# Kernel tuning notes

Measured on AMD Instinct MI355X. Metric: run time of the kernel, lower is better.

## Reference

```python
import jax, jax.numpy as jnp
import numpy as np

U = 359347   # user_num (hardcoded in source)
I = 292589   # item_num (hardcoded in source)
D = 64       # factor_num
NNZ = 4_000_000
B = 32768
LAM = 0.001  # lamada


def setup_inputs() -> dict:
    key = jax.random.key(0)
    ks = jax.random.split(key, 19)
    return {
        "ui_rows": jax.random.randint(ks[0], (NNZ,), 0, U, dtype=jnp.int32),
        "ui_cols": jax.random.randint(ks[1], (NNZ,), 0, I, dtype=jnp.int32),
        "ui_vals": jax.random.uniform(ks[2], (NNZ,), dtype=jnp.float32),
        "iu_vals": jax.random.uniform(ks[3], (NNZ,), dtype=jnp.float32),
        "d_i": jax.random.uniform(ks[4], (U,), dtype=jnp.float32),
        "d_j": jax.random.uniform(ks[5], (I,), dtype=jnp.float32),
        "embed_user": jax.random.normal(ks[6], (U, D), dtype=jnp.float32) * 0.01,
        "embed_item": jax.random.normal(ks[7], (I, D), dtype=jnp.float32) * 0.01,
        "add_w": jax.random.normal(ks[8], (1, 3), dtype=jnp.float32),
        "fw1": jax.random.normal(ks[9], (2 * D, D), dtype=jnp.float32) * (1.0 / np.sqrt(D)),
        "fb1": jax.random.normal(ks[10], (2 * D,), dtype=jnp.float32) * 0.01,
        "fw2": jax.random.normal(ks[11], (D, 2 * D), dtype=jnp.float32) * (1.0 / np.sqrt(2 * D)),
        "fb2": jax.random.normal(ks[12], (D,), dtype=jnp.float32) * 0.01,
        "user_bias": jax.random.normal(ks[13], (U, 1), dtype=jnp.float32) * 0.01,
        "item_bias": jax.random.normal(ks[14], (I, 1), dtype=jnp.float32) * 0.01,
        "avg_rating": jax.random.uniform(ks[15], (1,), dtype=jnp.float32) * 5.0,
        "user0": jax.random.randint(ks[16], (B,), 0, U, dtype=jnp.int32),
        "item_i0": jax.random.randint(ks[17], (B,), 0, I, dtype=jnp.int32),
        "ratings": jax.random.uniform(ks[18], (B,), dtype=jnp.float32) * 5.0,
    }


def _spmm(rows, cols, vals, x, num_rows):
    # sparse [num_rows, *] COO @ dense x : gather rows of x by col index,
    # scale by edge value, scatter-add into destination rows.
    return jax.ops.segment_sum(vals[:, None] * x[cols], rows, num_segments=num_rows)


def _leaky(x):
    return jnp.where(x > 0, x, 0.1 * x)


def _user_filter(x, fw1, fb1, fw2, fb2):
    h = _leaky(x @ fw1.T + fb1)
    return _leaky(h @ fw2.T + fb2)


def reference(ui_rows, ui_cols, ui_vals, iu_vals, d_i, d_j,
              embed_user, embed_item, add_w, fw1, fb1, fw2, fb2,
              user_bias, item_bias, avg_rating, user0, item_i0, ratings):
    ue, ie = embed_user, embed_item
    # layer 1: SpMM + degree-scaled residual + ReLU
    g1_u = jax.nn.relu(_spmm(ui_rows, ui_cols, ui_vals, ie, U) + ue * d_i[:, None])
    g1_i = jax.nn.relu(_spmm(ui_cols, ui_rows, iu_vals, ue, I) + ie * d_j[:, None])
    # layer 2
    g2_u = jax.nn.relu(_spmm(ui_rows, ui_cols, ui_vals, g1_i, U) + g1_u * d_i[:, None])
    g2_i = jax.nn.relu(_spmm(ui_cols, ui_rows, iu_vals, g1_u, I) + g1_i * d_j[:, None])
    # learned combination of the 3 layers: Linear(3,1) over the stacked axis
    w = add_w[0]  # [3]
    gcn_u = w[0] * ue + w[1] * g1_u + w[2] * g2_u   # [U, D]
    gcn_i = w[0] * ie + w[1] * g1_i + w[2] * g2_i   # [I, D]
    # batch lookup + shared filter MLP
    user = _user_filter(gcn_u[user0], fw1, fb1, fw2, fb2)      # [B, D]
    item = _user_filter(gcn_i[item_i0], fw1, fb1, fw2, fb2)    # [B, D]
    pred = (user * item).sum(-1) + user_bias[user0, 0] + item_bias[item_i0, 0] + avg_rating
    l2 = LAM * jnp.mean(gcn_u ** 2) + LAM * jnp.mean(gcn_i ** 2)
    loss2 = jnp.mean((pred - ratings) ** 2)
    return loss2 + l2
```

## Files before the change

kernel.cpp:

```cpp
#include <hip/hip_runtime.h>

#define U_NUM 359347
#define I_NUM 292589
#define DDIM  64
#define NNZ_N 4000000
#define BATCH 32768
#define LAM_F 0.001f
#define ACC_SLOTS 2048

#define EPB   4096
#define NBLK  ((NNZ_N + EPB - 1) / EPB)
#define NB_U  ((U_NUM + 1023) >> 10)
#define NB_I  ((I_NUM + 1023) >> 10)

__device__ __forceinline__ float leaky(float x) { return x > 0.f ? x : 0.1f * x; }

__device__ __forceinline__ unsigned short f2bf(float f) {
    unsigned b = __float_as_uint(f);
    b = (b + 0x7FFF + ((b >> 16) & 1)) >> 16;
    return (unsigned short)b;
}
__device__ __forceinline__ float bf2f(unsigned short u) {
    return __uint_as_float((unsigned)u << 16);
}
__device__ __forceinline__ float bflo(unsigned u) { return __uint_as_float(u << 16); }
__device__ __forceinline__ float bfhi(unsigned u) { return __uint_as_float(u & 0xffff0000u); }

__device__ __forceinline__ unsigned char f2fp8(float v) {
    v = fminf(fmaxf(v * 64.f, -440.f), 440.f);
    unsigned b = __float_as_uint(v * 0x1p-120f);
    unsigned sign = (b >> 24) & 0x80u;
    unsigned mag = b & 0x7fffffffu;
    mag += 0x7ffffu + ((mag >> 20) & 1u);
    return (unsigned char)(sign | ((mag >> 20) & 0x7fu));
}

#if __has_builtin(__builtin_amdgcn_cvt_f32_fp8)
#define FP8DEC(b) __builtin_amdgcn_cvt_f32_fp8((int)(b), 0)
#else
#define FP8DEC(b) (__uint_as_float(((unsigned)((b) & 0x80u) << 24) | \
                                   ((unsigned)((b) & 0x7fu) << 20)) * 0x1p120f)
#endif

__global__ __launch_bounds__(256) void f2bf8_k(
    const float4* __restrict__ in, ushort4* __restrict__ outb,
    uchar4* __restrict__ out8, size_t n4)
{
    size_t stride = (size_t)gridDim.x * 256;
    for (size_t i = (size_t)blockIdx.x * 256 + threadIdx.x; i < n4; i += stride) {
        float4 v = in[i];
        ushort4 o;
        o.x = f2bf(v.x); o.y = f2bf(v.y); o.z = f2bf(v.z); o.w = f2bf(v.w);
        outb[i] = o;
        uchar4 p;
        p.x = f2fp8(v.x); p.y = f2fp8(v.y); p.z = f2fp8(v.z); p.w = f2fp8(v.w);
        out8[i] = p;
    }
}

__global__ __launch_bounds__(256) void l1hist_k(
    const int* __restrict__ keys, int* __restrict__ gh, int nb)
{
    __shared__ int h[512];
    for (int i = threadIdx.x; i < nb; i += 256) h[i] = 0;
    __syncthreads();
    int base = blockIdx.x * EPB;
    int end = min(base + EPB, NNZ_N);
    for (int e = base + threadIdx.x; e < end; e += 256)
        atomicAdd(&h[keys[e] >> 10], 1);
    __syncthreads();
    for (int i = threadIdx.x; i < nb; i += 256)
        gh[i * NBLK + blockIdx.x] = h[i];
}

__global__ __launch_bounds__(256) void scan1_k(int* __restrict__ a, int n, int* __restrict__ bsum)
{
    __shared__ int s[256];
    int t = threadIdx.x;
    int base = blockIdx.x * 1024 + t * 4;
    int v[4];
#pragma unroll
    for (int j = 0; j < 4; ++j) v[j] = (base + j < n) ? a[base + j] : 0;
    s[t] = v[0] + v[1] + v[2] + v[3];
    __syncthreads();
    for (int off = 1; off < 256; off <<= 1) {
        int x = (t >= off) ? s[t - off] : 0;
        __syncthreads();
        s[t] += x;
        __syncthreads();
    }
    if (t == 255) bsum[blockIdx.x] = s[255];
    int run = (t > 0) ? s[t - 1] : 0;
#pragma unroll
    for (int j = 0; j < 4; ++j) {
        if (base + j < n) a[base + j] = run;
        run += v[j];
    }
}

__global__ __launch_bounds__(512) void scan2_k(int* __restrict__ bsum, int nb)
{
    __shared__ int s[512];
    int t = threadIdx.x;
    int v = (t < nb) ? bsum[t] : 0;
    s[t] = v;
    __syncthreads();
    for (int off = 1; off < 512; off <<= 1) {
        int x = (t >= off) ? s[t - off] : 0;
        __syncthreads();
        s[t] += x;
        __syncthreads();
    }
    if (t < nb) bsum[t] = s[t] - v;
}

__global__ __launch_bounds__(256) void scan3_k(int* __restrict__ a, int n,
                                               const int* __restrict__ bsum)
{
    int add = bsum[blockIdx.x];
    int base = blockIdx.x * 1024 + threadIdx.x * 4;
#pragma unroll
    for (int j = 0; j < 4; ++j)
        if (base + j < n) a[base + j] += add;
}

__global__ __launch_bounds__(256) void l1scatter_k(
    const int* __restrict__ keys, const int* __restrict__ gh, int nb,
    int2* __restrict__ out)
{
    __shared__ int cur[512];
    for (int i = threadIdx.x; i < nb; i += 256) cur[i] = gh[i * NBLK + blockIdx.x];
    __syncthreads();
    int base = blockIdx.x * EPB;
    int end = min(base + EPB, NNZ_N);
    for (int e = base + threadIdx.x; e < end; e += 256) {
        int k = keys[e];
        int pos = atomicAdd(&cur[k >> 10], 1);
        out[pos] = make_int2(k, e);
    }
}

__global__ __launch_bounds__(256) void l2sort_k(
    const int2* __restrict__ tmp, const int* __restrict__ gh, int nb,
    const int* __restrict__ colArr, const float* __restrict__ valArr,
    int* __restrict__ ptr, int nrows,
    int* __restrict__ ecol, unsigned short* __restrict__ eval)
{
    __shared__ int hist[1024];
    __shared__ int ssc[256];
    int b = blockIdx.x;
    int t = threadIdx.x;
    int bucket_base = gh[b * NBLK];
    int bucket_end  = (b == nb - 1) ? NNZ_N : gh[(b + 1) * NBLK];
    for (int i = t; i < 1024; i += 256) hist[i] = 0;
    __syncthreads();
    for (int e = bucket_base + t; e < bucket_end; e += 256)
        atomicAdd(&hist[tmp[e].x & 1023], 1);
    __syncthreads();
    int v0 = hist[t * 4], v1 = hist[t * 4 + 1], v2 = hist[t * 4 + 2], v3 = hist[t * 4 + 3];
    ssc[t] = v0 + v1 + v2 + v3;
    __syncthreads();
    for (int off = 1; off < 256; off <<= 1) {
        int x = (t >= off) ? ssc[t - off] : 0;
        __syncthreads();
        ssc[t] += x;
        __syncthreads();
    }
    int run = (t > 0) ? ssc[t - 1] : 0;
    int g0 = run, g1 = run + v0, g2 = g1 + v1, g3 = g2 + v2;
    hist[t * 4] = g0; hist[t * 4 + 1] = g1; hist[t * 4 + 2] = g2; hist[t * 4 + 3] = g3;
    int rbase = b << 10;
    if (rbase + t * 4 < nrows)     ptr[rbase + t * 4]     = bucket_base + g0;
    if (rbase + t * 4 + 1 < nrows) ptr[rbase + t * 4 + 1] = bucket_base + g1;
    if (rbase + t * 4 + 2 < nrows) ptr[rbase + t * 4 + 2] = bucket_base + g2;
    if (rbase + t * 4 + 3 < nrows) ptr[rbase + t * 4 + 3] = bucket_base + g3;
    if (b == nb - 1 && t == 0) ptr[nrows] = NNZ_N;
    __syncthreads();
    for (int e = bucket_base + t; e < bucket_end; e += 256) {
        int2 q = tmp[e];
        int pos = bucket_base + atomicAdd(&hist[q.x & 1023], 1);
        ecol[pos] = colArr[q.y];
        eval[pos] = f2bf(valArr[q.y] * 0.015625f);
    }
}

template <int MODE>
__global__ __launch_bounds__(256) void spmm_csr_k(
    const int* __restrict__ ptr, const int* __restrict__ ecol,
    const unsigned short* __restrict__ eval,
    const unsigned char* __restrict__ x8, const unsigned short* base,
    const float* __restrict__ deg, unsigned short* out, int nrows,
    unsigned char* __restrict__ out8,
    const unsigned short* embed, const float* __restrict__ add_w,
    float* __restrict__ accArr)
{
    int wv = threadIdx.x >> 6, lane = threadIdx.x & 63;
    int r = blockIdx.x * 4 + wv;
    __shared__ float ssum[4];
    if (r < nrows) {
        int s0 = __builtin_amdgcn_readfirstlane(ptr[r]);
        int e0 = __builtin_amdgcn_readfirstlane(ptr[r + 1]);
        float a0 = 0.f, a1 = 0.f, a2 = 0.f, a3 = 0.f;
        int k = s0;
        for (; k + 4 <= e0; k += 4) {
            int c0 = ecol[k], c1 = ecol[k + 1], c2 = ecol[k + 2], c3 = ecol[k + 3];
            float v0 = bf2f(eval[k]),     v1 = bf2f(eval[k + 1]);
            float v2 = bf2f(eval[k + 2]), v3 = bf2f(eval[k + 3]);
            unsigned char b0 = x8[(size_t)c0 * DDIM + lane];
            unsigned char b1 = x8[(size_t)c1 * DDIM + lane];
            unsigned char b2 = x8[(size_t)c2 * DDIM + lane];
            unsigned char b3 = x8[(size_t)c3 * DDIM + lane];
            a0 = fmaf(v0, FP8DEC(b0), a0);
            a1 = fmaf(v1, FP8DEC(b1), a1);
            a2 = fmaf(v2, FP8DEC(b2), a2);
            a3 = fmaf(v3, FP8DEC(b3), a3);
        }
        for (; k < e0; ++k)
            a0 = fmaf(bf2f(eval[k]), FP8DEC(x8[(size_t)ecol[k] * DDIM + lane]), a0);
        float acc = (a0 + a1) + (a2 + a3);
        float bb = bf2f(base[(size_t)r * DDIM + lane]);
        float o = fmaxf(fmaf(bb, deg[r], acc), 0.f);
        if (MODE == 0) {
            out[(size_t)r * DDIM + lane] = f2bf(o);
            out8[(size_t)r * DDIM + lane] = f2fp8(o);
        } else {
            float g = fmaf(add_w[0], bf2f(embed[(size_t)r * DDIM + lane]),
                           fmaf(add_w[1], bb, add_w[2] * o));
            out[(size_t)r * DDIM + lane] = f2bf(g);
            float sq = g * g;
            for (int off = 32; off; off >>= 1) sq += __shfl_down(sq, off);
            if (lane == 0) ssum[wv] = sq;
        }
    } else if (MODE == 1) {
        if (lane == 0) ssum[wv] = 0.f;
    }
    if (MODE == 1) {
        __syncthreads();
        if (threadIdx.x == 0)
            atomicAdd(&accArr[blockIdx.x & (ACC_SLOTS - 1)],
                      ssum[0] + ssum[1] + ssum[2] + ssum[3]);
    }
}

__global__ __launch_bounds__(256) void mlp_k(
    const int* __restrict__ user0, const int* __restrict__ item0,
    const unsigned short* __restrict__ gcnU, const unsigned short* __restrict__ gcnI,
    const float* __restrict__ fw1, const float* __restrict__ fb1,
    const float* __restrict__ fw2, const float* __restrict__ fb2,
    unsigned short* __restrict__ ou, unsigned short* __restrict__ oi)
{
    __shared__ unsigned short xs[64][72];
    __shared__ unsigned short w1s[128][68];
    __shared__ unsigned short w2s[64][140];
    __shared__ unsigned short hs[128][72];
    __shared__ float b1s[128];
    __shared__ float b2s[64];

    int t = threadIdx.x;
    int side = blockIdx.x >> 9;
    int tile = blockIdx.x & 511;
    const int* sel = side ? item0 : user0;
    const unsigned short* gcn = side ? gcnI : gcnU;
    unsigned short* outp = side ? oi : ou;

    {
        int r = t >> 2, c = t & 3;
        int idx = sel[tile * 64 + r];
        const ushort4* src = (const ushort4*)(gcn + (size_t)idx * 64 + c * 16);
        ushort4 v0 = src[0], v1 = src[1], v2 = src[2], v3 = src[3];
        int k0 = c * 16;
        xs[k0 +  0][r] = v0.x; xs[k0 +  1][r] = v0.y; xs[k0 +  2][r] = v0.z; xs[k0 +  3][r] = v0.w;
        xs[k0 +  4][r] = v1.x; xs[k0 +  5][r] = v1.y; xs[k0 +  6][r] = v1.z; xs[k0 +  7][r] = v1.w;
        xs[k0 +  8][r] = v2.x; xs[k0 +  9][r] = v2.y; xs[k0 + 10][r] = v2.z; xs[k0 + 11][r] = v2.w;
        xs[k0 + 12][r] = v3.x; xs[k0 + 13][r] = v3.y; xs[k0 + 14][r] = v3.z; xs[k0 + 15][r] = v3.w;
    }
#pragma unroll
    for (int i = 0; i < 8; ++i) {
        int flat = i * 1024 + t * 4;
        float4 w = *(const float4*)(fw1 + flat);
        int o = flat >> 6, k = flat & 63;
        *(unsigned*)&w1s[o][k]     = (unsigned)f2bf(w.x) | ((unsigned)f2bf(w.y) << 16);
        *(unsigned*)&w1s[o][k + 2] = (unsigned)f2bf(w.z) | ((unsigned)f2bf(w.w) << 16);
        float4 u = *(const float4*)(fw2 + flat);
        int o2 = flat >> 7, k2 = flat & 127;
        *(unsigned*)&w2s[o2][k2]     = (unsigned)f2bf(u.x) | ((unsigned)f2bf(u.y) << 16);
        *(unsigned*)&w2s[o2][k2 + 2] = (unsigned)f2bf(u.z) | ((unsigned)f2bf(u.w) << 16);
    }
    if (t < 128) b1s[t] = fb1[t];
    if (t < 64)  b2s[t] = fb2[t];
    __syncthreads();

    int sg = t & 15, og = t >> 4;

    float acc[4][8];
#pragma unroll
    for (int i = 0; i < 4; ++i)
#pragma unroll
        for (int j = 0; j < 8; ++j) acc[i][j] = 0.f;

    for (int kc = 0; kc < 64; kc += 4) {
        uint2 xp0 = *(const uint2*)&xs[kc    ][sg * 4];
        uint2 xp1 = *(const uint2*)&xs[kc + 1][sg * 4];
        uint2 xp2 = *(const uint2*)&xs[kc + 2][sg * 4];
        uint2 xp3 = *(const uint2*)&xs[kc + 3][sg * 4];
        float x0[4] = { bflo(xp0.x), bfhi(xp0.x), bflo(xp0.y), bfhi(xp0.y) };
        float x1[4] = { bflo(xp1.x), bfhi(xp1.x), bflo(xp1.y), bfhi(xp1.y) };
        float x2[4] = { bflo(xp2.x), bfhi(xp2.x), bflo(xp2.y), bfhi(xp2.y) };
        float x3[4] = { bflo(xp3.x), bfhi(xp3.x), bflo(xp3.y), bfhi(xp3.y) };
#pragma unroll
        for (int j = 0; j < 8; ++j) {
            uint2 wp = *(const uint2*)&w1s[og * 8 + j][kc];
            float w0 = bflo(wp.x), w1v = bfhi(wp.x), w2v = bflo(wp.y), w3v = bfhi(wp.y);
#pragma unroll
            for (int i = 0; i < 4; ++i) {
                acc[i][j] = fmaf(x0[i], w0,  acc[i][j]);
                acc[i][j] = fmaf(x1[i], w1v, acc[i][j]);
                acc[i][j] = fmaf(x2[i], w2v, acc[i][j]);
                acc[i][j] = fmaf(x3[i], w3v, acc[i][j]);
            }
        }
    }
#pragma unroll
    for (int j = 0; j < 8; ++j) {
        int o = og * 8 + j;
        float b = b1s[o];
        float h0 = leaky(acc[0][j] + b), h1 = leaky(acc[1][j] + b);
        float h2 = leaky(acc[2][j] + b), h3 = leaky(acc[3][j] + b);
        *(unsigned*)&hs[o][sg * 4]     = (unsigned)f2bf(h0) | ((unsigned)f2bf(h1) << 16);
        *(unsigned*)&hs[o][sg * 4 + 2] = (unsigned)f2bf(h2) | ((unsigned)f2bf(h3) << 16);
    }
    __syncthreads();

    float acc2[4][4];
#pragma unroll
    for (int i = 0; i < 4; ++i)
#pragma unroll
        for (int j = 0; j < 4; ++j) acc2[i][j] = 0.f;

    for (int kc = 0; kc < 128; kc += 4) {
        uint2 hp0 = *(const uint2*)&hs[kc    ][sg * 4];
        uint2 hp1 = *(const uint2*)&hs[kc + 1][sg * 4];
        uint2 hp2 = *(const uint2*)&hs[kc + 2][sg * 4];
        uint2 hp3 = *(const uint2*)&hs[kc + 3][sg * 4];
        float h0[4] = { bflo(hp0.x), bfhi(hp0.x), bflo(hp0.y), bfhi(hp0.y) };
        float h1[4] = { bflo(hp1.x), bfhi(hp1.x), bflo(hp1.y), bfhi(hp1.y) };
        float h2[4] = { bflo(hp2.x), bfhi(hp2.x), bflo(hp2.y), bfhi(hp2.y) };
        float h3[4] = { bflo(hp3.x), bfhi(hp3.x), bflo(hp3.y), bfhi(hp3.y) };
#pragma unroll
        for (int j = 0; j < 4; ++j) {
            uint2 wp = *(const uint2*)&w2s[og * 4 + j][kc];
            float w0 = bflo(wp.x), w1v = bfhi(wp.x), w2v = bflo(wp.y), w3v = bfhi(wp.y);
#pragma unroll
            for (int i = 0; i < 4; ++i) {
                acc2[i][j] = fmaf(h0[i], w0,  acc2[i][j]);
                acc2[i][j] = fmaf(h1[i], w1v, acc2[i][j]);
                acc2[i][j] = fmaf(h2[i], w2v, acc2[i][j]);
                acc2[i][j] = fmaf(h3[i], w3v, acc2[i][j]);
            }
        }
    }
#pragma unroll
    for (int i = 0; i < 4; ++i) {
        float o0 = leaky(acc2[i][0] + b2s[og * 4 + 0]);
        float o1 = leaky(acc2[i][1] + b2s[og * 4 + 1]);
        float o2 = leaky(acc2[i][2] + b2s[og * 4 + 2]);
        float o3 = leaky(acc2[i][3] + b2s[og * 4 + 3]);
        uint2 pp;
        pp.x = (unsigned)f2bf(o0) | ((unsigned)f2bf(o1) << 16);
        pp.y = (unsigned)f2bf(o2) | ((unsigned)f2bf(o3) << 16);
        *(uint2*)(outp + ((size_t)(tile * 64 + sg * 4 + i) * 64 + og * 4)) = pp;
    }
}

__global__ __launch_bounds__(256) void dot_sse_k(
    const unsigned short* __restrict__ ou, const unsigned short* __restrict__ oi,
    const int* __restrict__ user0, const int* __restrict__ item0,
    const float* __restrict__ ub, const float* __restrict__ ib,
    const float* __restrict__ avg, const float* __restrict__ ratings,
    float* __restrict__ sse)
{
    int g = blockIdx.x * 256 + threadIdx.x;
    int b = g >> 2, q = g & 3;
    const uint4* pu = (const uint4*)(ou + (size_t)b * 64 + q * 16);
    const uint4* pi = (const uint4*)(oi + (size_t)b * 64 + q * 16);
    uint4 a0 = pu[0], a1 = pu[1];
    uint4 c0 = pi[0], c1 = pi[1];
    float s = 0.f;
#define DOTP(ua, uc) { s = fmaf(bflo(ua), bflo(uc), s); s = fmaf(bfhi(ua), bfhi(uc), s); }
    DOTP(a0.x, c0.x) DOTP(a0.y, c0.y) DOTP(a0.z, c0.z) DOTP(a0.w, c0.w)
    DOTP(a1.x, c1.x) DOTP(a1.y, c1.y) DOTP(a1.z, c1.z) DOTP(a1.w, c1.w)
#undef DOTP
    s += __shfl_xor(s, 1);
    s += __shfl_xor(s, 2);
    float contrib = 0.f;
    if (q == 0) {
        float pred = s + ub[user0[b]] + ib[item0[b]] + avg[0];
        float d = pred - ratings[b];
        contrib = d * d;
    }
    for (int off = 32; off; off >>= 1) contrib += __shfl_down(contrib, off);
    __shared__ float wsum[4];
    int lane = threadIdx.x & 63, wv = threadIdx.x >> 6;
    if (lane == 0) wsum[wv] = contrib;
    __syncthreads();
    if (threadIdx.x == 0)
        atomicAdd(sse, wsum[0] + wsum[1] + wsum[2] + wsum[3]);
}

__global__ __launch_bounds__(256) void finalize2_k(
    const float* __restrict__ accU, const float* __restrict__ accI,
    const float* __restrict__ sse, float* __restrict__ out)
{
    int t = threadIdx.x;
    float su = 0.f, si = 0.f;
    for (int i = t; i < ACC_SLOTS; i += 256) { su += accU[i]; si += accI[i]; }
    for (int off = 32; off; off >>= 1) {
        su += __shfl_down(su, off);
        si += __shfl_down(si, off);
    }
    __shared__ float s[8];
    int wv = t >> 6, lane = t & 63;
    if (lane == 0) { s[wv] = su; s[wv + 4] = si; }
    __syncthreads();
    if (t == 0) {
        float SU = s[0] + s[1] + s[2] + s[3];
        float SI = s[4] + s[5] + s[6] + s[7];
        out[0] = sse[0] / (float)BATCH
               + LAM_F * (SU / (float)((double)U_NUM * 64.0))
               + LAM_F * (SI / (float)((double)I_NUM * 64.0));
    }
}


extern "C" void kernel_launch(void* const* d_in, const int* in_sizes, int n_in,
                              void* d_out, int out_size, void* d_ws, size_t ws_size,
                              hipStream_t stream)
{
    const int*   ui_rows = (const int*)d_in[0];
    const int*   ui_cols = (const int*)d_in[1];
    const float* ui_vals = (const float*)d_in[2];
    const float* iu_vals = (const float*)d_in[3];
    const float* d_i     = (const float*)d_in[4];
    const float* d_j     = (const float*)d_in[5];
    const float* eu      = (const float*)d_in[6];
    const float* ei      = (const float*)d_in[7];
    const float* add_w   = (const float*)d_in[8];
    const float* fw1     = (const float*)d_in[9];
    const float* fb1     = (const float*)d_in[10];
    const float* fw2     = (const float*)d_in[11];
    const float* fb2     = (const float*)d_in[12];
    const float* ub      = (const float*)d_in[13];
    const float* ib      = (const float*)d_in[14];
    const float* avg     = (const float*)d_in[15];
    const int*   user0   = (const int*)d_in[16];
    const int*   item0   = (const int*)d_in[17];
    const float* ratings = (const float*)d_in[18];

    const size_t U64 = (size_t)U_NUM * DDIM;
    const size_t I64 = (size_t)I_NUM * DDIM;

    int*            ecol_u = (int*)d_ws;
    unsigned short* eval_u = (unsigned short*)(ecol_u + NNZ_N);
    int*            ecol_i = (int*)(eval_u + NNZ_N);
    unsigned short* eval_i = (unsigned short*)(ecol_i + NNZ_N);
    int2* tmpb  = (int2*)(eval_i + NNZ_N);
    unsigned char*  g1u_f8 = (unsigned char*)tmpb;
    unsigned short* ou_bf  = (unsigned short*)(g1u_f8 + ((U64 + 15) & ~15ull));
    unsigned short* oi_bf  = ou_bf + (size_t)BATCH * 64;
    int*  gh    = (int*)(tmpb + NNZ_N);
    int*  bsum  = gh + (size_t)NB_U * NBLK;
    int*  ptr_u = bsum + 512;
    int*  ptr_i = ptr_u + (U_NUM + 1);
    float* accU = (float*)(ptr_i + (I_NUM + 1));
    float* accI = accU + ACC_SLOTS;
    float* sse  = accI + ACC_SLOTS;
    unsigned short* eu_bf  = (unsigned short*)(sse + 4);
    unsigned short* ei_bf  = eu_bf + U64;
    unsigned short* g1u_bf = ei_bf + I64;
    unsigned short* g1i_bf = g1u_bf + U64;
    unsigned char*  eu_f8  = (unsigned char*)(g1i_bf + I64);
    unsigned char*  ei_f8  = eu_f8 + U64;
    unsigned char*  g1i_f8 = ei_f8 + I64;
    (void)ws_size;

    dim3 blk(256);
    int gu = (U_NUM + 3) / 4, gi = (I_NUM + 3) / 4;

    hipMemsetAsync(accU, 0, (2 * ACC_SLOTS + 4) * sizeof(float), stream);

    f2bf8_k<<<2048, blk, 0, stream>>>((const float4*)eu, (ushort4*)eu_bf,
                                      (uchar4*)eu_f8, U64 / 4);
    f2bf8_k<<<2048, blk, 0, stream>>>((const float4*)ei, (ushort4*)ei_bf,
                                      (uchar4*)ei_f8, I64 / 4);

    {
        int n = NB_U * NBLK;
        int nb1 = (n + 1023) / 1024;
        l1hist_k<<<NBLK, blk, 0, stream>>>(ui_rows, gh, NB_U);
        scan1_k<<<nb1, blk, 0, stream>>>(gh, n, bsum);
        scan2_k<<<1, 512, 0, stream>>>(bsum, nb1);
        scan3_k<<<nb1, blk, 0, stream>>>(gh, n, bsum);
        l1scatter_k<<<NBLK, blk, 0, stream>>>(ui_rows, gh, NB_U, tmpb);
        l2sort_k<<<NB_U, blk, 0, stream>>>(tmpb, gh, NB_U, ui_cols, ui_vals,
                                           ptr_u, U_NUM, ecol_u, eval_u);
    }
    {
        int n = NB_I * NBLK;
        int nb1 = (n + 1023) / 1024;
        l1hist_k<<<NBLK, blk, 0, stream>>>(ui_cols, gh, NB_I);
        scan1_k<<<nb1, blk, 0, stream>>>(gh, n, bsum);
        scan2_k<<<1, 512, 0, stream>>>(bsum, nb1);
        scan3_k<<<nb1, blk, 0, stream>>>(gh, n, bsum);
        l1scatter_k<<<NBLK, blk, 0, stream>>>(ui_cols, gh, NB_I, tmpb);
        l2sort_k<<<NB_I, blk, 0, stream>>>(tmpb, gh, NB_I, ui_rows, iu_vals,
                                           ptr_i, I_NUM, ecol_i, eval_i);
    }

    spmm_csr_k<0><<<gu, blk, 0, stream>>>(ptr_u, ecol_u, eval_u, ei_f8, eu_bf, d_i,
                                          g1u_bf, U_NUM, g1u_f8, nullptr, nullptr, nullptr);
    spmm_csr_k<0><<<gi, blk, 0, stream>>>(ptr_i, ecol_i, eval_i, eu_f8, ei_bf, d_j,
                                          g1i_bf, I_NUM, g1i_f8, nullptr, nullptr, nullptr);
    spmm_csr_k<1><<<gi, blk, 0, stream>>>(ptr_i, ecol_i, eval_i, g1u_f8, g1i_bf, d_j,
                                          ei_bf, I_NUM, nullptr, ei_bf, add_w, accI);
    spmm_csr_k<1><<<gu, blk, 0, stream>>>(ptr_u, ecol_u, eval_u, g1i_f8, g1u_bf, d_i,
                                          g1u_bf, U_NUM, nullptr, eu_bf, add_w, accU);

    mlp_k<<<1024, blk, 0, stream>>>(user0, item0, g1u_bf, ei_bf,
                                    fw1, fb1, fw2, fb2, ou_bf, oi_bf);
    dot_sse_k<<<BATCH * 4 / 256, blk, 0, stream>>>(ou_bf, oi_bf, user0, item0,
                                                   ub, ib, avg, ratings, sse);
    finalize2_k<<<1, blk, 0, stream>>>(accU, accI, sse, (float*)d_out);
}
```

Measured before the change: 1.323 ms.

## Merge user/item preprocessing and SpMM launches, carry col/val through scatter

Independent user-side and item-side kernels are merged into single launches that pick their side by block index. This covers the embedding conversion, histogram, the three scan stages and both SpMM layers. The first-level scatter now writes the column index and the pre-scaled bf16 value alongside the key. The second-level sort then copies them sequentially instead of doing random gathers into the original column and value arrays. The SpMM inner loop is unrolled to 8 edges to keep more gather loads in flight. The cost is an extra temporary value buffer, larger per-side histogram and workspace arrays, and some per-block selection overhead and register pressure.

```diff
diff --git a/kernel.cpp b/kernel.cpp
--- a/kernel.cpp
+++ b/kernel.cpp
@@ -34,7 +34,6 @@
     mag += 0x7ffffu + ((mag >> 20) & 1u);
     return (unsigned char)(sign | ((mag >> 20) & 0x7fu));
 }
-
 #if __has_builtin(__builtin_amdgcn_cvt_f32_fp8)
 #define FP8DEC(b) __builtin_amdgcn_cvt_f32_fp8((int)(b), 0)
 #else
@@ -43,41 +42,58 @@
 #endif
 
 __global__ __launch_bounds__(256) void f2bf8_k(
-    const float4* __restrict__ in, ushort4* __restrict__ outb,
-    uchar4* __restrict__ out8, size_t n4)
+    const float4* __restrict__ inU, ushort4* __restrict__ obU, uchar4* __restrict__ o8U,
+    const float4* __restrict__ inI, ushort4* __restrict__ obI, uchar4* __restrict__ o8I,
+    size_t nU4, size_t total4)
 {
     size_t stride = (size_t)gridDim.x * 256;
-    for (size_t i = (size_t)blockIdx.x * 256 + threadIdx.x; i < n4; i += stride) {
-        float4 v = in[i];
+    for (size_t i = (size_t)blockIdx.x * 256 + threadIdx.x; i < total4; i += stride) {
+        const float4* in; ushort4* ob; uchar4* o8; size_t j;
+        if (i < nU4) { in = inU; ob = obU; o8 = o8U; j = i; }
+        else         { in = inI; ob = obI; o8 = o8I; j = i - nU4; }
+        float4 v = in[j];
         ushort4 o;
         o.x = f2bf(v.x); o.y = f2bf(v.y); o.z = f2bf(v.z); o.w = f2bf(v.w);
-        outb[i] = o;
+        ob[j] = o;
         uchar4 p;
         p.x = f2fp8(v.x); p.y = f2fp8(v.y); p.z = f2fp8(v.z); p.w = f2fp8(v.w);
-        out8[i] = p;
-    }
-}
-
-__global__ __launch_bounds__(256) void l1hist_k(
-    const int* __restrict__ keys, int* __restrict__ gh, int nb)
+        o8[j] = p;
+    }
+}
+
+__global__ __launch_bounds__(256) void hist2_k(
+    const int* __restrict__ rows, const int* __restrict__ cols,
+    int* __restrict__ gh_u, int* __restrict__ gh_i)
 {
     __shared__ int h[512];
+    int sideB = blockIdx.x >= NBLK;
+    int blk = sideB ? blockIdx.x - NBLK : blockIdx.x;
+    const int* keys = sideB ? cols : rows;
+    int nb = sideB ? NB_I : NB_U;
+    int* gh = sideB ? gh_i : gh_u;
     for (int i = threadIdx.x; i < nb; i += 256) h[i] = 0;
     __syncthreads();
-    int base = blockIdx.x * EPB;
+    int base = blk * EPB;
     int end = min(base + EPB, NNZ_N);
     for (int e = base + threadIdx.x; e < end; e += 256)
         atomicAdd(&h[keys[e] >> 10], 1);
     __syncthreads();
     for (int i = threadIdx.x; i < nb; i += 256)
-        gh[i * NBLK + blockIdx.x] = h[i];
-}
-
-__global__ __launch_bounds__(256) void scan1_k(int* __restrict__ a, int n, int* __restrict__ bsum)
+        gh[i * NBLK + blk] = h[i];
+}
+
+__global__ __launch_bounds__(256) void scan1m_k(
+    int* __restrict__ aU, int nUe, int* __restrict__ bsU, int nb1U,
+    int* __restrict__ aI, int nIe, int* __restrict__ bsI)
 {
     __shared__ int s[256];
+    int sideB = (int)blockIdx.x >= nb1U;
+    int blk = sideB ? blockIdx.x - nb1U : blockIdx.x;
+    int* a = sideB ? aI : aU;
+    int n = sideB ? nIe : nUe;
+    int* bsum = sideB ? bsI : bsU;
     int t = threadIdx.x;
-    int base = blockIdx.x * 1024 + t * 4;
+    int base = blk * 1024 + t * 4;
     int v[4];
 #pragma unroll
     for (int j = 0; j < 4; ++j) v[j] = (base + j < n) ? a[base + j] : 0;
@@ -89,7 +105,7 @@
         s[t] += x;
         __syncthreads();
     }
-    if (t == 255) bsum[blockIdx.x] = s[255];
+    if (t == 255) bsum[blk] = s[255];
     int run = (t > 0) ? s[t - 1] : 0;
 #pragma unroll
     for (int j = 0; j < 4; ++j) {
@@ -98,9 +114,12 @@
     }
 }
 
-__global__ __launch_bounds__(512) void scan2_k(int* __restrict__ bsum, int nb)
+__global__ __launch_bounds__(512) void scan2m_k(
+    int* __restrict__ bsU, int nbU, int* __restrict__ bsI, int nbI)
 {
     __shared__ int s[512];
+    int* bsum = blockIdx.x ? bsI : bsU;
+    int nb = blockIdx.x ? nbI : nbU;
     int t = threadIdx.x;
     int v = (t < nb) ? bsum[t] : 0;
     s[t] = v;
@@ -114,19 +133,25 @@
     if (t < nb) bsum[t] = s[t] - v;
 }
 
-__global__ __launch_bounds__(256) void scan3_k(int* __restrict__ a, int n,
-                                               const int* __restrict__ bsum)
-{
-    int add = bsum[blockIdx.x];
-    int base = blockIdx.x * 1024 + threadIdx.x * 4;
+__global__ __launch_bounds__(256) void scan3m_k(
+    int* __restrict__ aU, int nUe, const int* __restrict__ bsU, int nb1U,
+    int* __restrict__ aI, int nIe, const int* __restrict__ bsI)
+{
+    int sideB = (int)blockIdx.x >= nb1U;
+    int blk = sideB ? blockIdx.x - nb1U : blockIdx.x;
+    int* a = sideB ? aI : aU;
+    int n = sideB ? nIe : nUe;
+    int add = (sideB ? bsI : bsU)[blk];
+    int base = blk * 1024 + threadIdx.x * 4;
 #pragma unroll
     for (int j = 0; j < 4; ++j)
         if (base + j < n) a[base + j] += add;
 }
 
-__global__ __launch_bounds__(256) void l1scatter_k(
-    const int* __restrict__ keys, const int* __restrict__ gh, int nb,
-    int2* __restrict__ out)
+__global__ __launch_bounds__(256) void scat_k(
+    const int* __restrict__ keys, const int* __restrict__ cols,
+    const float* __restrict__ vals, const int* __restrict__ gh, int nb,
+    int2* __restrict__ tmpb, unsigned short* __restrict__ tmpv)
 {
     __shared__ int cur[512];
     for (int i = threadIdx.x; i < nb; i += 256) cur[i] = gh[i * NBLK + blockIdx.x];
@@ -136,14 +161,14 @@
     for (int e = base + threadIdx.x; e < end; e += 256) {
         int k = keys[e];
         int pos = atomicAdd(&cur[k >> 10], 1);
-        out[pos] = make_int2(k, e);
+        tmpb[pos] = make_int2(k, cols[e]);
+        tmpv[pos] = f2bf(vals[e] * 0.015625f);
     }
 }
 
 __global__ __launch_bounds__(256) void l2sort_k(
-    const int2* __restrict__ tmp, const int* __restrict__ gh, int nb,
-    const int* __restrict__ colArr, const float* __restrict__ valArr,
-    int* __restrict__ ptr, int nrows,
+    const int2* __restrict__ tmpb, const unsigned short* __restrict__ tmpv,
+    const int* __restrict__ gh, int nb, int* __restrict__ ptr, int nrows,
     int* __restrict__ ecol, unsigned short* __restrict__ eval)
 {
     __shared__ int hist[1024];
@@ -155,7 +180,7 @@
     for (int i = t; i < 1024; i += 256) hist[i] = 0;
     __syncthreads();
     for (int e = bucket_base + t; e < bucket_end; e += 256)
-        atomicAdd(&hist[tmp[e].x & 1023], 1);
+        atomicAdd(&hist[tmpb[e].x & 1023], 1);
     __syncthreads();
     int v0 = hist[t * 4], v1 = hist[t * 4 + 1], v2 = hist[t * 4 + 2], v3 = hist[t * 4 + 3];
     ssc[t] = v0 + v1 + v2 + v3;
@@ -177,43 +202,75 @@
     if (b == nb - 1 && t == 0) ptr[nrows] = NNZ_N;
     __syncthreads();
     for (int e = bucket_base + t; e < bucket_end; e += 256) {
-        int2 q = tmp[e];
+        int2 q = tmpb[e];
         int pos = bucket_base + atomicAdd(&hist[q.x & 1023], 1);
-        ecol[pos] = colArr[q.y];
-        eval[pos] = f2bf(valArr[q.y] * 0.015625f);
+        ecol[pos] = q.y;
+        eval[pos] = tmpv[e];
     }
 }
 
 template <int MODE>
-__global__ __launch_bounds__(256) void spmm_csr_k(
-    const int* __restrict__ ptr, const int* __restrict__ ecol,
-    const unsigned short* __restrict__ eval,
-    const unsigned char* __restrict__ x8, const unsigned short* base,
-    const float* __restrict__ deg, unsigned short* out, int nrows,
-    unsigned char* __restrict__ out8,
-    const unsigned short* embed, const float* __restrict__ add_w,
-    float* __restrict__ accArr)
+__global__ __launch_bounds__(256) void spmm_dual_k(
+    int gA,
+    const int* __restrict__ ptrA, const int* __restrict__ ecolA, const unsigned short* __restrict__ evalA,
+    const unsigned char* __restrict__ x8A, const unsigned short* baseA, const float* __restrict__ degA,
+    unsigned short* outA, int nA, unsigned char* __restrict__ out8A,
+    const unsigned short* embedA, float* __restrict__ accA,
+    const int* __restrict__ ptrB, const int* __restrict__ ecolB, const unsigned short* __restrict__ evalB,
+    const unsigned char* __restrict__ x8B, const unsigned short* baseB, const float* __restrict__ degB,
+    unsigned short* outB, int nB, unsigned char* __restrict__ out8B,
+    const unsigned short* embedB, float* __restrict__ accB,
+    const float* __restrict__ add_w)
 {
     int wv = threadIdx.x >> 6, lane = threadIdx.x & 63;
-    int r = blockIdx.x * 4 + wv;
+    int bid = blockIdx.x;
+    int sideB = bid >= gA;
+    int lb = sideB ? bid - gA : bid;
+    const int* ptr = sideB ? ptrB : ptrA;
+    const int* ecol = sideB ? ecolB : ecolA;
+    const unsigned short* eval = sideB ? evalB : evalA;
+    const unsigned char* x8 = sideB ? x8B : x8A;
+    const unsigned short* base = sideB ? baseB : baseA;
+    const float* deg = sideB ? degB : degA;
+    unsigned short* out = sideB ? outB : outA;
+    int nrows = sideB ? nB : nA;
     __shared__ float ssum[4];
+    int r = lb * 4 + wv;
     if (r < nrows) {
         int s0 = __builtin_amdgcn_readfirstlane(ptr[r]);
         int e0 = __builtin_amdgcn_readfirstlane(ptr[r + 1]);
         float a0 = 0.f, a1 = 0.f, a2 = 0.f, a3 = 0.f;
         int k = s0;
-        for (; k + 4 <= e0; k += 4) {
-            int c0 = ecol[k], c1 = ecol[k + 1], c2 = ecol[k + 2], c3 = ecol[k + 3];
-            float v0 = bf2f(eval[k]),     v1 = bf2f(eval[k + 1]);
-            float v2 = bf2f(eval[k + 2]), v3 = bf2f(eval[k + 3]);
+        for (; k + 8 <= e0; k += 8) {
+            int c0 = ecol[k],     c1 = ecol[k + 1], c2 = ecol[k + 2], c3 = ecol[k + 3];
+            int c4 = ecol[k + 4], c5 = ecol[k + 5], c6 = ecol[k + 6], c7 = ecol[k + 7];
             unsigned char b0 = x8[(size_t)c0 * DDIM + lane];
             unsigned char b1 = x8[(size_t)c1 * DDIM + lane];
             unsigned char b2 = x8[(size_t)c2 * DDIM + lane];
             unsigned char b3 = x8[(size_t)c3 * DDIM + lane];
-            a0 = fmaf(v0, FP8DEC(b0), a0);
-            a1 = fmaf(v1, FP8DEC(b1), a1);
-            a2 = fmaf(v2, FP8DEC(b2), a2);
-            a3 = fmaf(v3, FP8DEC(b3), a3);
+            unsigned char b4 = x8[(size_t)c4 * DDIM + lane];
+            unsigned char b5 = x8[(size_t)c5 * DDIM + lane];
+            unsigned char b6 = x8[(size_t)c6 * DDIM + lane];
+            unsigned char b7 = x8[(size_t)c7 * DDIM + lane];
+            a0 = fmaf(bf2f(eval[k]),     FP8DEC(b0), a0);
+            a1 = fmaf(bf2f(eval[k + 1]), FP8DEC(b1), a1);
+            a2 = fmaf(bf2f(eval[k + 2]), FP8DEC(b2), a2);
+            a3 = fmaf(bf2f(eval[k + 3]), FP8DEC(b3), a3);
+            a0 = fmaf(bf2f(eval[k + 4]), FP8DEC(b4), a0);
+            a1 = fmaf(bf2f(eval[k + 5]), FP8DEC(b5), a1);
+            a2 = fmaf(bf2f(eval[k + 6]), FP8DEC(b6), a2);
+            a3 = fmaf(bf2f(eval[k + 7]), FP8DEC(b7), a3);
+        }
+        for (; k + 4 <= e0; k += 4) {
+            int c0 = ecol[k], c1 = ecol[k + 1], c2 = ecol[k + 2], c3 = ecol[k + 3];
+            unsigned char b0 = x8[(size_t)c0 * DDIM + lane];
+            unsigned char b1 = x8[(size_t)c1 * DDIM + lane];
+            unsigned char b2 = x8[(size_t)c2 * DDIM + lane];
+            unsigned char b3 = x8[(size_t)c3 * DDIM + lane];
+            a0 = fmaf(bf2f(eval[k]),     FP8DEC(b0), a0);
+            a1 = fmaf(bf2f(eval[k + 1]), FP8DEC(b1), a1);
+            a2 = fmaf(bf2f(eval[k + 2]), FP8DEC(b2), a2);
+            a3 = fmaf(bf2f(eval[k + 3]), FP8DEC(b3), a3);
         }
         for (; k < e0; ++k)
             a0 = fmaf(bf2f(eval[k]), FP8DEC(x8[(size_t)ecol[k] * DDIM + lane]), a0);
@@ -222,8 +279,9 @@
         float o = fmaxf(fmaf(bb, deg[r], acc), 0.f);
         if (MODE == 0) {
             out[(size_t)r * DDIM + lane] = f2bf(o);
-            out8[(size_t)r * DDIM + lane] = f2fp8(o);
+            (sideB ? out8B : out8A)[(size_t)r * DDIM + lane] = f2fp8(o);
         } else {
+            const unsigned short* embed = sideB ? embedB : embedA;
             float g = fmaf(add_w[0], bf2f(embed[(size_t)r * DDIM + lane]),
                            fmaf(add_w[1], bb, add_w[2] * o));
             out[(size_t)r * DDIM + lane] = f2bf(g);
@@ -237,7 +295,7 @@
     if (MODE == 1) {
         __syncthreads();
         if (threadIdx.x == 0)
-            atomicAdd(&accArr[blockIdx.x & (ACC_SLOTS - 1)],
+            atomicAdd(&(sideB ? accB : accA)[lb & (ACC_SLOTS - 1)],
                       ssum[0] + ssum[1] + ssum[2] + ssum[3]);
     }
 }
@@ -463,13 +521,16 @@
     unsigned short* eval_u = (unsigned short*)(ecol_u + NNZ_N);
     int*            ecol_i = (int*)(eval_u + NNZ_N);
     unsigned short* eval_i = (unsigned short*)(ecol_i + NNZ_N);
-    int2* tmpb  = (int2*)(eval_i + NNZ_N);
+    int2*           tmpb   = (int2*)(eval_i + NNZ_N);
+    unsigned short* tmpv   = (unsigned short*)(tmpb + NNZ_N);
     unsigned char*  g1u_f8 = (unsigned char*)tmpb;
     unsigned short* ou_bf  = (unsigned short*)(g1u_f8 + ((U64 + 15) & ~15ull));
     unsigned short* oi_bf  = ou_bf + (size_t)BATCH * 64;
-    int*  gh    = (int*)(tmpb + NNZ_N);
-    int*  bsum  = gh + (size_t)NB_U * NBLK;
-    int*  ptr_u = bsum + 512;
+    int*  gh_u  = (int*)(tmpv + NNZ_N);
+    int*  gh_i  = gh_u + (size_t)NB_U * NBLK;
+    int*  bsumU = gh_i + (size_t)NB_I * NBLK;
+    int*  bsumI = bsumU + 512;
+    int*  ptr_u = bsumI + 512;
     int*  ptr_i = ptr_u + (U_NUM + 1);
     float* accU = (float*)(ptr_i + (I_NUM + 1));
     float* accI = accU + ACC_SLOTS;
@@ -485,45 +546,34 @@
 
     dim3 blk(256);
     int gu = (U_NUM + 3) / 4, gi = (I_NUM + 3) / 4;
-
-    hipMemsetAsync(accU, 0, (2 * ACC_SLOTS + 4) * sizeof(float), stream);
-
-    f2bf8_k<<<2048, blk, 0, stream>>>((const float4*)eu, (ushort4*)eu_bf,
-                                      (uchar4*)eu_f8, U64 / 4);
-    f2bf8_k<<<2048, blk, 0, stream>>>((const float4*)ei, (ushort4*)ei_bf,
-                                      (uchar4*)ei_f8, I64 / 4);
-
-    {
-        int n = NB_U * NBLK;
-        int nb1 = (n + 1023) / 1024;
-        l1hist_k<<<NBLK, blk, 0, stream>>>(ui_rows, gh, NB_U);
-        scan1_k<<<nb1, blk, 0, stream>>>(gh, n, bsum);
-        scan2_k<<<1, 512, 0, stream>>>(bsum, nb1);
-        scan3_k<<<nb1, blk, 0, stream>>>(gh, n, bsum);
-        l1scatter_k<<<NBLK, blk, 0, stream>>>(ui_rows, gh, NB_U, tmpb);
-        l2sort_k<<<NB_U, blk, 0, stream>>>(tmpb, gh, NB_U, ui_cols, ui_vals,
-                                           ptr_u, U_NUM, ecol_u, eval_u);
-    }
-    {
-        int n = NB_I * NBLK;
-        int nb1 = (n + 1023) / 1024;
-        l1hist_k<<<NBLK, blk, 0, stream>>>(ui_cols, gh, NB_I);
-        scan1_k<<<nb1, blk, 0, stream>>>(gh, n, bsum);
-        scan2_k<<<1, 512, 0, stream>>>(bsum, nb1);
-        scan3_k<<<nb1, blk, 0, stream>>>(gh, n, bsum);
-        l1scatter_k<<<NBLK, blk, 0, stream>>>(ui_cols, gh, NB_I, tmpb);
-        l2sort_k<<<NB_I, blk, 0, stream>>>(tmpb, gh, NB_I, ui_rows, iu_vals,
-                                           ptr_i, I_NUM, ecol_i, eval_i);
-    }
-
-    spmm_csr_k<0><<<gu, blk, 0, stream>>>(ptr_u, ecol_u, eval_u, ei_f8, eu_bf, d_i,
-                                          g1u_bf, U_NUM, g1u_f8, nullptr, nullptr, nullptr);
-    spmm_csr_k<0><<<gi, blk, 0, stream>>>(ptr_i, ecol_i, eval_i, eu_f8, ei_bf, d_j,
-                                          g1i_bf, I_NUM, g1i_f8, nullptr, nullptr, nullptr);
-    spmm_csr_k<1><<<gi, blk, 0, stream>>>(ptr_i, ecol_i, eval_i, g1u_f8, g1i_bf, d_j,
-                                          ei_bf, I_NUM, nullptr, ei_bf, add_w, accI);
-    spmm_csr_k<1><<<gu, blk, 0, stream>>>(ptr_u, ecol_u, eval_u, g1i_f8, g1u_bf, d_i,
-                                          g1u_bf, U_NUM, nullptr, eu_bf, add_w, accU);
+    int nUe = NB_U * NBLK, nIe = NB_I * NBLK;
+    int nb1U = (nUe + 1023) / 1024, nb1I = (nIe + 1023) / 1024;
+
+    size_t meta_bytes = ((char*)(sse + 4)) - (char*)gh_u;
+    hipMemsetAsync(gh_u, 0, meta_bytes, stream);
+
+    f2bf8_k<<<2048, blk, 0, stream>>>((const float4*)eu, (ushort4*)eu_bf, (uchar4*)eu_f8,
+                                      (const float4*)ei, (ushort4*)ei_bf, (uchar4*)ei_f8,
+                                      U64 / 4, (U64 + I64) / 4);
+
+    hist2_k<<<2 * NBLK, blk, 0, stream>>>(ui_rows, ui_cols, gh_u, gh_i);
+    scan1m_k<<<nb1U + nb1I, blk, 0, stream>>>(gh_u, nUe, bsumU, nb1U, gh_i, nIe, bsumI);
+    scan2m_k<<<2, 512, 0, stream>>>(bsumU, nb1U, bsumI, nb1I);
+    scan3m_k<<<nb1U + nb1I, blk, 0, stream>>>(gh_u, nUe, bsumU, nb1U, gh_i, nIe, bsumI);
+
+    scat_k<<<NBLK, blk, 0, stream>>>(ui_rows, ui_cols, ui_vals, gh_u, NB_U, tmpb, tmpv);
+    l2sort_k<<<NB_U, blk, 0, stream>>>(tmpb, tmpv, gh_u, NB_U, ptr_u, U_NUM, ecol_u, eval_u);
+    scat_k<<<NBLK, blk, 0, stream>>>(ui_cols, ui_rows, iu_vals, gh_i, NB_I, tmpb, tmpv);
+    l2sort_k<<<NB_I, blk, 0, stream>>>(tmpb, tmpv, gh_i, NB_I, ptr_i, I_NUM, ecol_i, eval_i);
+
+    spmm_dual_k<0><<<gu + gi, blk, 0, stream>>>(gu,
+        ptr_u, ecol_u, eval_u, ei_f8, eu_bf, d_i, g1u_bf, U_NUM, g1u_f8, nullptr, nullptr,
+        ptr_i, ecol_i, eval_i, eu_f8, ei_bf, d_j, g1i_bf, I_NUM, g1i_f8, nullptr, nullptr,
+        nullptr);
+    spmm_dual_k<1><<<gi + gu, blk, 0, stream>>>(gi,
+        ptr_i, ecol_i, eval_i, g1u_f8, g1i_bf, d_j, ei_bf, I_NUM, nullptr, ei_bf, accI,
+        ptr_u, ecol_u, eval_u, g1i_f8, g1u_bf, d_i, g1u_bf, U_NUM, nullptr, eu_bf, accU,
+        add_w);
 
     mlp_k<<<1024, blk, 0, stream>>>(user0, item0, g1u_bf, ei_bf,
                                     fw1, fb1, fw2, fb2, ou_bf, oi_bf);
```

After: 1.228 ms. -7.2%, faster.
